# Performance work log

Measured on AMD Instinct MI355X. Metric: run time of the kernel, lower is better.

Reference implementation:

```python
import jax, jax.numpy as jnp
import numpy as np

B, H, W, C = 16, 32, 32, 512
L, CT = 77, 512
NH, HD = 8, 64
G = 32          # GroupNorm groups
EPS = 1e-6      # flax GroupNorm default epsilon
NEG = -1e10


def group_norm(x, scale, bias):
    # flax GroupNorm on [b, n, c]: stats over (n, channels-within-group) per (b, group)
    b, n, c = x.shape
    xg = x.reshape(b, n, G, c // G)
    mu = xg.mean(axis=(1, 3), keepdims=True)
    var = xg.var(axis=(1, 3), keepdims=True)
    xg = (xg - mu) * jax.lax.rsqrt(var + EPS)
    return xg.reshape(b, n, c) * scale + bias


def setup_inputs() -> dict:
    key = jax.random.key(0)
    ks = jax.random.split(key, 8)
    w = lambda k, shape: jax.random.normal(k, shape, jnp.float32) * 0.02
    return {
        "inputs": jax.random.normal(ks[0], (B, H, W, C), jnp.float32),
        "text_enc": jax.random.normal(ks[1], (B, L, CT), jnp.float32),
        "text_mask": jnp.ones((B, L), jnp.int32),
        "gn_q_scale": jnp.ones((C,), jnp.float32),
        "gn_q_bias": jnp.zeros((C,), jnp.float32),
        "gn_kv_scale": jnp.ones((C,), jnp.float32),
        "gn_kv_bias": jnp.zeros((C,), jnp.float32),
        "gn_t_scale": jnp.ones((CT,), jnp.float32),
        "gn_t_bias": jnp.zeros((CT,), jnp.float32),
        "Wq": w(ks[2], (C, NH, HD)),
        "Wk_self": w(ks[3], (C, NH, HD)),
        "Wv_self": w(ks[4], (C, NH, HD)),
        "Wk_cross": w(ks[5], (CT, NH, HD)),
        "Wv_cross": w(ks[6], (CT, NH, HD)),
        "Wout": w(ks[7], (NH, HD, C)),
    }


def reference(inputs, text_enc, text_mask,
              gn_q_scale, gn_q_bias, gn_kv_scale, gn_kv_bias,
              gn_t_scale, gn_t_bias,
              Wq, Wk_self, Wv_self, Wk_cross, Wv_cross, Wout):
    b, h, w, c = inputs.shape
    n = h * w
    x = inputs.reshape(b, n, c)

    x_q = group_norm(x, gn_q_scale, gn_q_bias)
    x_kv = group_norm(x, gn_kv_scale, gn_kv_bias)
    t = group_norm(text_enc, gn_t_scale, gn_t_bias)

    # q/k/v projections; fused: KV = concat(self-KV from image, cross-KV from text)
    scale = jnp.asarray(1.0 / np.sqrt(HD), inputs.dtype)
    q = jnp.einsum('bqc,chd->bqhd', x_q, Wq) * scale  # scale_attn_logits
    k = jnp.concatenate([jnp.einsum('bkc,chd->bkhd', x_kv, Wk_self),
                         jnp.einsum('blc,chd->blhd', t, Wk_cross)], axis=1)
    v = jnp.concatenate([jnp.einsum('bkc,chd->bkhd', x_kv, Wv_self),
                         jnp.einsum('blc,chd->blhd', t, Wv_cross)], axis=1)

    # make_attention_mask(ones[b,n], concat(ones[b,n], text_mask)) -> [b,1,n,n+l];
    # query mask is all ones so only the KV mask matters.
    kv_mask = jnp.concatenate(
        [jnp.ones((b, n), jnp.bool_), text_mask > 0], axis=1)  # [b, n+l]

    logits = jnp.einsum('bqhd,bkhd->bhqk', q, k)  # [b, nh, n, n+l]
    logits = jnp.where(kv_mask[:, None, None, :], logits, jnp.asarray(NEG, logits.dtype))
    probs = jax.nn.softmax(logits, axis=-1)
    attn = jnp.einsum('bhqk,bkhd->bqhd', probs, v)
    out = jnp.einsum('bqhd,hdc->bqc', attn, Wout)
    return out.reshape(b, h, w, c) + inputs
```

## Files before the change

kernel.cpp:

```cpp
#include <hip/hip_runtime.h>
#include <hip/hip_bf16.h>

typedef __hip_bfloat16 bf16;
typedef __attribute__((ext_vector_type(8))) short short8;
typedef __attribute__((ext_vector_type(4))) float f32x4;
typedef __attribute__((ext_vector_type(16))) float f32x16;
#define MFMA16(a, b, c) __builtin_amdgcn_mfma_f32_16x16x32_bf16(a, b, c, 0, 0, 0)
#define MFMA32(a, b, c) __builtin_amdgcn_mfma_f32_32x32x16_bf16(a, b, c, 0, 0, 0)

#define BB   16
#define CCH  512
#define NN   1024
#define LLT  77
#define LPAD 128
#define NHH  8
#define HDD  64
#define GGN  32
#define NKV  1101
#define KVP  1152

__device__ __forceinline__ unsigned short f2bu(float f){
  bf16 h = __float2bfloat16(f);
  return *reinterpret_cast<unsigned short*>(&h);
}

__device__ __forceinline__ unsigned pk2(float lo, float hi){
  unsigned r;
  asm("v_cvt_pk_bf16_f32 %0, %1, %2" : "=v"(r) : "v"(lo), "v"(hi));
  return r;
}

__device__ __forceinline__ float fexp2(float x){
  float r;
  asm("v_exp_f32 %0, %1" : "=v"(r) : "v"(x));
  return r;
}

__device__ __forceinline__ void pl32swap(unsigned &a, unsigned &b){
  asm("v_permlane32_swap_b32 %0, %1" : "+v"(a), "+v"(b));
}

__global__ __launch_bounds__(256) void gn_stats_kernel(
    const float* __restrict__ ximg, const float* __restrict__ xtxt,
    float* __restrict__ stats )
{
  int isimg = blockIdx.x < 512;
  int bid = blockIdx.x & 511;
  int b = bid >> 5, g = bid & 31;
  int npos = isimg ? NN : LLT;
  const float* xb = (isimg ? ximg : xtxt) + (size_t)b * npos * CCH + g * 16;
  int tot4 = npos * 4;
  float s = 0.f, s2 = 0.f;
  for (int e = threadIdx.x; e < tot4; e += 256){
    int n = e >> 2, cq = (e & 3) * 4;
    float4 v = *(const float4*)(xb + (size_t)n * CCH + cq);
    s  += v.x + v.y + v.z + v.w;
    s2 += v.x * v.x + v.y * v.y + v.z * v.z + v.w * v.w;
  }
  __shared__ float sh1[256], sh2[256];
  sh1[threadIdx.x] = s; sh2[threadIdx.x] = s2;
  __syncthreads();
  for (int off = 128; off > 0; off >>= 1){
    if (threadIdx.x < off){
      sh1[threadIdx.x] += sh1[threadIdx.x + off];
      sh2[threadIdx.x] += sh2[threadIdx.x + off];
    }
    __syncthreads();
  }
  if (threadIdx.x == 0){
    float inv = 1.f / (float)(npos * 16);
    float m = sh1[0] * inv;
    float var = sh2[0] * inv - m * m;
    float* mu = stats + (isimg ? 0 : 1024);
    mu[bid] = m;
    mu[512 + bid] = rsqrtf(var + 1e-6f);
  }
}

__global__ __launch_bounds__(256) void prep_weights_kernel(
    const float* __restrict__ W0, const float* __restrict__ W1,
    const float* __restrict__ W2, const float* __restrict__ W3,
    const float* __restrict__ W4, const float* __restrict__ W5,
    bf16* __restrict__ Wt)
{
  int wsel = blockIdx.z;
  const float* W = wsel == 0 ? W0 : wsel == 1 ? W1 : wsel == 2 ? W2 :
                   wsel == 3 ? W3 : wsel == 4 ? W4 : W5;
  bf16* dst = Wt + (size_t)wsel * CCH * CCH;
  int n0 = blockIdx.x * 64, k0 = blockIdx.y * 64;

  __shared__ alignas(16) float Ws[64][68];
  int r = threadIdx.x >> 2, c = (threadIdx.x & 3) * 16;
  const float* src = W + (size_t)(k0 + r) * CCH + n0 + c;
  *(float4*)&Ws[r][c]      = *(const float4*)(src);
  *(float4*)&Ws[r][c + 4]  = *(const float4*)(src + 4);
  *(float4*)&Ws[r][c + 8]  = *(const float4*)(src + 8);
  *(float4*)&Ws[r][c + 12] = *(const float4*)(src + 12);
  __syncthreads();

  int nr = threadIdx.x >> 2, kc = (threadIdx.x & 3) * 16;
  uint4 o0, o1;
  o0.x = pk2(Ws[kc + 0][nr],  Ws[kc + 1][nr]);
  o0.y = pk2(Ws[kc + 2][nr],  Ws[kc + 3][nr]);
  o0.z = pk2(Ws[kc + 4][nr],  Ws[kc + 5][nr]);
  o0.w = pk2(Ws[kc + 6][nr],  Ws[kc + 7][nr]);
  o1.x = pk2(Ws[kc + 8][nr],  Ws[kc + 9][nr]);
  o1.y = pk2(Ws[kc + 10][nr], Ws[kc + 11][nr]);
  o1.z = pk2(Ws[kc + 12][nr], Ws[kc + 13][nr]);
  o1.w = pk2(Ws[kc + 14][nr], Ws[kc + 15][nr]);
  bf16* d = dst + (size_t)(n0 + nr) * CCH + k0 + kc;
  *(uint4*)d = o0;
  *(uint4*)(d + 8) = o1;
}

__global__ __launch_bounds__(256) void norm_all_kernel(
    const float* __restrict__ x, const float* __restrict__ t,
    const float* __restrict__ stats,
    const float* __restrict__ gqs, const float* __restrict__ gqb,
    const float* __restrict__ gks, const float* __restrict__ gkb,
    const float* __restrict__ gts, const float* __restrict__ gtb,
    bf16* __restrict__ Xq, bf16* __restrict__ Xkv, bf16* __restrict__ Tn)
{
  if (blockIdx.x < 4096){
    size_t e = ((size_t)blockIdx.x * 256 + threadIdx.x) * 8;
    int b  = (int)(e >> 19);
    int ch = (int)(e & 511);
    int g  = ch >> 4;
    float m = stats[b * GGN + g], r = stats[512 + b * GGN + g];
    float4 x0 = *(const float4*)(x + e);
    float4 x1 = *(const float4*)(x + e + 4);
    float4 sq0 = *(const float4*)(gqs + ch), sq1 = *(const float4*)(gqs + ch + 4);
    float4 bq0 = *(const float4*)(gqb + ch), bq1 = *(const float4*)(gqb + ch + 4);
    float4 sk0 = *(const float4*)(gks + ch), sk1 = *(const float4*)(gks + ch + 4);
    float4 bk0 = *(const float4*)(gkb + ch), bk1 = *(const float4*)(gkb + ch + 4);
    float xs[8] = {x0.x,x0.y,x0.z,x0.w,x1.x,x1.y,x1.z,x1.w};
    float sqv[8] = {sq0.x,sq0.y,sq0.z,sq0.w,sq1.x,sq1.y,sq1.z,sq1.w};
    float bqv[8] = {bq0.x,bq0.y,bq0.z,bq0.w,bq1.x,bq1.y,bq1.z,bq1.w};
    float skv[8] = {sk0.x,sk0.y,sk0.z,sk0.w,sk1.x,sk1.y,sk1.z,sk1.w};
    float bkv[8] = {bk0.x,bk0.y,bk0.z,bk0.w,bk1.x,bk1.y,bk1.z,bk1.w};
    float q[8], k[8];
    #pragma unroll
    for (int j = 0; j < 8; j++){
      float nx = (xs[j] - m) * r;
      q[j] = (nx * sqv[j] + bqv[j]) * 0.18033688f;
      k[j] = nx * skv[j] + bkv[j];
    }
    uint4 oq, ok;
    oq.x = pk2(q[0], q[1]); oq.y = pk2(q[2], q[3]);
    oq.z = pk2(q[4], q[5]); oq.w = pk2(q[6], q[7]);
    ok.x = pk2(k[0], k[1]); ok.y = pk2(k[2], k[3]);
    ok.z = pk2(k[4], k[5]); ok.w = pk2(k[6], k[7]);
    *(uint4*)(Xq + e)  = oq;
    *(uint4*)(Xkv + e) = ok;
  } else {
    size_t e = ((size_t)(blockIdx.x - 4096) * 256 + threadIdx.x) * 8;
    int b  = (int)(e >> 16);
    int rem = (int)(e & 65535);
    int l  = rem >> 9;
    int ch = rem & 511;
    uint4 o;
    if (l < LLT){
      int g = ch >> 4;
      float m = stats[1024 + b * GGN + g], r = stats[1536 + b * GGN + g];
      const float* src = t + ((size_t)b * LLT + l) * CCH + ch;
      float4 x0 = *(const float4*)src, x1 = *(const float4*)(src + 4);
      float4 s0 = *(const float4*)(gts + ch), s1 = *(const float4*)(gts + ch + 4);
      float4 b0 = *(const float4*)(gtb + ch), b1 = *(const float4*)(gtb + ch + 4);
      float xs[8] = {x0.x,x0.y,x0.z,x0.w,x1.x,x1.y,x1.z,x1.w};
      float sv[8] = {s0.x,s0.y,s0.z,s0.w,s1.x,s1.y,s1.z,s1.w};
      float bv[8] = {b0.x,b0.y,b0.z,b0.w,b1.x,b1.y,b1.z,b1.w};
      float w[8];
      #pragma unroll
      for (int j = 0; j < 8; j++) w[j] = (xs[j] - m) * r * sv[j] + bv[j];
      o.x = pk2(w[0], w[1]); o.y = pk2(w[2], w[3]);
      o.z = pk2(w[4], w[5]); o.w = pk2(w[6], w[7]);
    } else {
      o = make_uint4(0, 0, 0, 0);
    }
    *(uint4*)(Tn + e) = o;
  }
}

__global__ __launch_bounds__(256) void proj_self_mfma(
    const bf16* __restrict__ Xq, const bf16* __restrict__ Xkv,
    const bf16* __restrict__ Wt,
    bf16* __restrict__ Qo, bf16* __restrict__ Ko, bf16* __restrict__ Vo)
{
  const int tid  = threadIdx.x;
  const int wave = tid >> 6, lane = tid & 63;
  const int l16 = lane & 15, quad = lane >> 4;
  const int wr = wave >> 1, wc = wave & 1;
  const int bx = blockIdx.x;
  const int ct = bx >> 7;
  const int rt = bx & 127;
  const int mat = ct >> 2;
  const int cm0 = (ct & 3) * 128;
  const int b  = rt >> 3;
  const int n0 = (rt & 7) * 128;

  __shared__ bf16 T[4][64][72];

  const bf16* A  = (mat == 0) ? Xq : Xkv;
  const bf16* Bw = Wt + (size_t)mat * CCH * CCH + (size_t)cm0 * CCH;

  f32x4 acc[4][4];
  #pragma unroll
  for (int rf = 0; rf < 4; rf++)
    #pragma unroll
    for (int cf = 0; cf < 4; cf++) acc[rf][cf] = (f32x4){0.f,0.f,0.f,0.f};

  const int sr = tid >> 2, sc = (tid & 3) * 16;
  const bf16* pa0 = A  + ((size_t)b * NN + n0 + sr) * CCH + sc;
  const bf16* pa1 = pa0 + (size_t)64 * CCH;
  const bf16* pb0 = Bw + (size_t)sr * CCH + sc;
  const bf16* pb1 = pb0 + (size_t)64 * CCH;

  uint4 rA0a = *(const uint4*)pa0, rA0b = *(const uint4*)(pa0 + 8);
  uint4 rA1a = *(const uint4*)pa1, rA1b = *(const uint4*)(pa1 + 8);
  uint4 rB0a = *(const uint4*)pb0, rB0b = *(const uint4*)(pb0 + 8);
  uint4 rB1a = *(const uint4*)pb1, rB1b = *(const uint4*)(pb1 + 8);

  for (int kt = 0; kt < 8; kt++){
    *(uint4*)&T[0][sr][sc] = rA0a;  *(uint4*)&T[0][sr][sc + 8] = rA0b;
    *(uint4*)&T[1][sr][sc] = rA1a;  *(uint4*)&T[1][sr][sc + 8] = rA1b;
    *(uint4*)&T[2][sr][sc] = rB0a;  *(uint4*)&T[2][sr][sc + 8] = rB0b;
    *(uint4*)&T[3][sr][sc] = rB1a;  *(uint4*)&T[3][sr][sc + 8] = rB1b;
    if (kt < 7){
      const int k1 = (kt + 1) * 64;
      rA0a = *(const uint4*)(pa0 + k1);  rA0b = *(const uint4*)(pa0 + k1 + 8);
      rA1a = *(const uint4*)(pa1 + k1);  rA1b = *(const uint4*)(pa1 + k1 + 8);
      rB0a = *(const uint4*)(pb0 + k1);  rB0b = *(const uint4*)(pb0 + k1 + 8);
      rB1a = *(const uint4*)(pb1 + k1);  rB1b = *(const uint4*)(pb1 + k1 + 8);
    }
    __syncthreads();

    short8 af[4][2];
    #pragma unroll
    for (int rf = 0; rf < 4; rf++){
      af[rf][0] = *(const short8*)&T[wr][rf * 16 + l16][quad * 8];
      af[rf][1] = *(const short8*)&T[wr][rf * 16 + l16][32 + quad * 8];
    }
    #pragma unroll
    for (int cf = 0; cf < 4; cf++){
      const short8 b0 = *(const short8*)&T[2 + wc][cf * 16 + l16][quad * 8];
      const short8 b1 = *(const short8*)&T[2 + wc][cf * 16 + l16][32 + quad * 8];
      #pragma unroll
      for (int rf = 0; rf < 4; rf++){
        acc[rf][cf] = MFMA16(af[rf][0], b0, acc[rf][cf]);
        acc[rf][cf] = MFMA16(af[rf][1], b1, acc[rf][cf]);
      }
    }
    __syncthreads();
  }

  if (mat < 2){
    bf16* Out = (mat == 0) ? Qo : Ko;
    const int stride = (mat == 0) ? NN : KVP;
    #pragma unroll
    for (int cf = 0; cf < 4; cf++){
      const int cm = cm0 + wc * 64 + cf * 16 + l16;
      const int h = cm >> 6, d = cm & 63;
      #pragma unroll
      for (int rf = 0; rf < 4; rf++)
        #pragma unroll
        for (int r = 0; r < 4; r++){
          const int n = n0 + wr * 64 + rf * 16 + quad * 4 + r;
          Out[(((size_t)b * NHH + h) * stride + n) * HDD + d] =
              __float2bfloat16(acc[rf][cf][r]);
        }
    }
  } else {
    bf16 (*Tw)[72] = T[wave];
    #pragma unroll
    for (int cf = 0; cf < 4; cf++)
      #pragma unroll
      for (int rf = 0; rf < 4; rf++)
        #pragma unroll
        for (int r = 0; r < 4; r++)
          Tw[cf * 16 + l16][rf * 16 + quad * 4 + r] =
              __float2bfloat16(acc[rf][cf][r]);
    __syncthreads();
    const int h  = (cm0 + wc * 64) >> 6;
    const int nb = n0 + wr * 64;
    const int dl = lane >> 2, cseg = (lane & 3) * 16;
    #pragma unroll
    for (int k2 = 0; k2 < 4; k2++){
      const int d = dl + k2 * 16;
      bf16* vd = Vo + (((size_t)b * NHH + h) * HDD + d) * KVP + nb + cseg;
      *(uint4*)vd       = *(const uint4*)&Tw[d][cseg];
      *(uint4*)(vd + 8) = *(const uint4*)&Tw[d][cseg + 8];
    }
  }
}

__global__ __launch_bounds__(256) void proj_cross_mfma(
    const bf16* __restrict__ Tn, const bf16* __restrict__ Wt,
    bf16* __restrict__ Ko, bf16* __restrict__ Vo)
{
  const int tid  = threadIdx.x;
  const int wave = tid >> 6, lane = tid & 63;
  const int l16 = lane & 15, quad = lane >> 4;
  const int h  = blockIdx.x;
  const int l0 = blockIdx.y * 64;
  const int b  = blockIdx.z;

  __shared__ bf16 At[64][72];
  __shared__ bf16 Bk[64][72], Bv[64][72];

  const bf16* Wkc = Wt + 3 * CCH * CCH;
  const bf16* Wvc = Wt + 4 * CCH * CCH;

  f32x4 sk[4], sv[4];
  #pragma unroll
  for (int nt = 0; nt < 4; nt++){
    sk[nt] = (f32x4){0.f,0.f,0.f,0.f};
    sv[nt] = (f32x4){0.f,0.f,0.f,0.f};
  }

  const int sr = tid >> 2, sc = (tid & 3) * 16;
  const bf16* p_a  = Tn  + ((size_t)b * LPAD + l0 + sr) * CCH + sc;
  const bf16* p_bk = Wkc + (size_t)(h * 64 + sr) * CCH + sc;
  const bf16* p_bv = Wvc + (size_t)(h * 64 + sr) * CCH + sc;

  uint4 ra0 = *(const uint4*)p_a,   ra1 = *(const uint4*)(p_a + 8);
  uint4 rk0 = *(const uint4*)p_bk,  rk1 = *(const uint4*)(p_bk + 8);
  uint4 rv0 = *(const uint4*)p_bv,  rv1 = *(const uint4*)(p_bv + 8);

  for (int kt = 0; kt < 8; kt++){
    *(uint4*)&At[sr][sc]     = ra0;  *(uint4*)&At[sr][sc + 8] = ra1;
    *(uint4*)&Bk[sr][sc]     = rk0;  *(uint4*)&Bk[sr][sc + 8] = rk1;
    *(uint4*)&Bv[sr][sc]     = rv0;  *(uint4*)&Bv[sr][sc + 8] = rv1;
    if (kt < 7){
      const int k1 = (kt + 1) * 64;
      ra0 = *(const uint4*)(p_a + k1);   ra1 = *(const uint4*)(p_a + k1 + 8);
      rk0 = *(const uint4*)(p_bk + k1);  rk1 = *(const uint4*)(p_bk + k1 + 8);
      rv0 = *(const uint4*)(p_bv + k1);  rv1 = *(const uint4*)(p_bv + k1 + 8);
    }
    __syncthreads();

    const short8 a0 = *(const short8*)&At[wave * 16 + l16][quad * 8];
    const short8 a1 = *(const short8*)&At[wave * 16 + l16][32 + quad * 8];
    #pragma unroll
    for (int nt = 0; nt < 4; nt++){
      const short8 bk0 = *(const short8*)&Bk[nt * 16 + l16][quad * 8];
      const short8 bk1 = *(const short8*)&Bk[nt * 16 + l16][32 + quad * 8];
      sk[nt] = MFMA16(a0, bk0, sk[nt]);
      sk[nt] = MFMA16(a1, bk1, sk[nt]);
      const short8 bv0 = *(const short8*)&Bv[nt * 16 + l16][quad * 8];
      const short8 bv1 = *(const short8*)&Bv[nt * 16 + l16][32 + quad * 8];
      sv[nt] = MFMA16(a0, bv0, sv[nt]);
      sv[nt] = MFMA16(a1, bv1, sv[nt]);
    }
    __syncthreads();
  }

  #pragma unroll
  for (int r = 0; r < 4; r++){
    int kvrow = NN + l0 + wave * 16 + quad * 4 + r;
    bf16* kd = Ko + (((size_t)b * NHH + h) * KVP + kvrow) * HDD + l16;
    #pragma unroll
    for (int nt = 0; nt < 4; nt++)
      kd[nt * 16] = __float2bfloat16(sk[nt][r]);
  }

  __syncthreads();
  #pragma unroll
  for (int nt = 0; nt < 4; nt++)
    #pragma unroll
    for (int r = 0; r < 4; r++)
      Bk[nt * 16 + l16][wave * 16 + quad * 4 + r] = __float2bfloat16(sv[nt][r]);
  __syncthreads();
  {
    int d = tid >> 2, c = (tid & 3) * 16;
    bf16* vd = Vo + (((size_t)b * NHH + h) * HDD + d) * KVP + NN + l0 + c;
    *(uint4*)vd       = *(const uint4*)&Bk[d][c];
    *(uint4*)(vd + 8) = *(const uint4*)&Bk[d][c + 8];
  }
}

__global__ __launch_bounds__(256, 4) void attn_mfma_kernel(
    const bf16* __restrict__ Q, const bf16* __restrict__ K,
    const bf16* __restrict__ Vt, const int* __restrict__ tmask,
    bf16* __restrict__ Ao)
{
  const int tid  = threadIdx.x;
  const int wave = tid >> 6;
  const int lane = tid & 63;
  const int l31  = lane & 31;
  const int hi   = lane >> 5;
  const int bx = blockIdx.x;
  const int q0 = (bx >> 7) * 128;
  const int g  = bx & 127;
  const int h  = g & 7;
  const int b  = g >> 3;

  __shared__ alignas(16) bf16 KV[2][2][64][72];

  const bf16* qp = Q + (((size_t)b * NHH + h) * NN + q0 + wave * 32 + l31) * HDD + hi * 8;
  short8 qf[4];
  qf[0] = *(const short8*)(qp);
  qf[1] = *(const short8*)(qp + 16);
  qf[2] = *(const short8*)(qp + 32);
  qf[3] = *(const short8*)(qp + 48);

  union { unsigned u[4]; short8 s8; } ones;
  ones.u[0] = 0x3F803F80u; ones.u[1] = 0x3F803F80u;
  ones.u[2] = 0x3F803F80u; ones.u[3] = 0x3F803F80u;

  f32x16 zf;
  #pragma unroll
  for (int i = 0; i < 16; i++) zf[i] = 0.f;

  f32x16 o_acc[2], l_acc;
  #pragma unroll
  for (int dt = 0; dt < 2; dt++)
    #pragma unroll
    for (int i = 0; i < 16; i++) o_acc[dt][i] = 0.f;
  #pragma unroll
  for (int i = 0; i < 16; i++) l_acc[i] = 0.f;

  const size_t kbase = ((size_t)b * NHH + h) * KVP;
  const size_t vbase = ((size_t)b * NHH + h) * (size_t)HDD * KVP;

  const int sr = tid >> 2;
  const int sc = (tid & 3) * 16;
  const bf16* kp = K  + (kbase + sr) * HDD + sc;
  const bf16* vp = Vt + vbase + (size_t)sr * KVP + sc;

  uint4 kr0 = *(const uint4*)kp, kr1 = *(const uint4*)(kp + 8);
  uint4 vr0 = *(const uint4*)vp, vr1 = *(const uint4*)(vp + 8);
  *(uint4*)&KV[0][0][sr][sc]     = kr0;
  *(uint4*)&KV[0][0][sr][sc + 8] = kr1;
  *(uint4*)&KV[0][1][sr][sc]     = vr0;
  *(uint4*)&KV[0][1][sr][sc + 8] = vr1;
  kr0 = *(const uint4*)(kp + 4096); kr1 = *(const uint4*)(kp + 4096 + 8);
  vr0 = *(const uint4*)(vp + 64);   vr1 = *(const uint4*)(vp + 64 + 8);
  __syncthreads();

  for (int kt = 0; kt < 18; kt++){
    const int cur = kt & 1;
    if (kt + 1 < 18){
      *(uint4*)&KV[cur ^ 1][0][sr][sc]     = kr0;
      *(uint4*)&KV[cur ^ 1][0][sr][sc + 8] = kr1;
      *(uint4*)&KV[cur ^ 1][1][sr][sc]     = vr0;
      *(uint4*)&KV[cur ^ 1][1][sr][sc + 8] = vr1;
    }
    if (kt + 2 < 18){
      const size_t ko = (size_t)(kt + 2) * 4096;
      const int    vo = (kt + 2) * 64;
      kr0 = *(const uint4*)(kp + ko); kr1 = *(const uint4*)(kp + ko + 8);
      vr0 = *(const uint4*)(vp + vo); vr1 = *(const uint4*)(vp + vo + 8);
    }

    const bf16 (*Ks)[72] = KV[cur][0];
    const bf16 (*Vs)[72] = KV[cur][1];
    const int kv0 = kt * 64;

    #pragma unroll
    for (int t = 0; t < 2; t++){
      const short8 kf0 = *(const short8*)&Ks[t * 32 + l31][hi * 8];
      const short8 kf1 = *(const short8*)&Ks[t * 32 + l31][16 + hi * 8];
      const short8 kf2 = *(const short8*)&Ks[t * 32 + l31][32 + hi * 8];
      const short8 kf3 = *(const short8*)&Ks[t * 32 + l31][48 + hi * 8];
      __builtin_amdgcn_s_setprio(1);
      f32x16 s = MFMA32(kf0, qf[0], zf);
      s = MFMA32(kf1, qf[1], s);
      s = MFMA32(kf2, qf[2], s);
      s = MFMA32(kf3, qf[3], s);
      __builtin_amdgcn_s_setprio(0);

      if (kv0 + 64 > NN){
        #pragma unroll
        for (int r = 0; r < 16; r++){
          int idx = kv0 - NN + t * 32 + (r & 3) + 8 * (r >> 2) + 4 * hi;
          int ci = idx < LLT ? idx : LLT - 1;
          float rep = (idx < LLT)
                        ? (tmask[b * LLT + ci] > 0 ? 1e30f : -1e10f)
                        : -1e30f;
          s[r] = fminf(s[r], rep);
        }
      }

      #pragma unroll
      for (int r = 0; r < 16; r++) s[r] = fexp2(s[r]);

      unsigned w0 = pk2(s[0],  s[1]),  w1 = pk2(s[2],  s[3]);
      unsigned w2 = pk2(s[4],  s[5]),  w3 = pk2(s[6],  s[7]);
      unsigned w4 = pk2(s[8],  s[9]),  w5 = pk2(s[10], s[11]);
      unsigned w6 = pk2(s[12], s[13]), w7 = pk2(s[14], s[15]);
      pl32swap(w0, w2);
      pl32swap(w1, w3);
      pl32swap(w4, w6);
      pl32swap(w5, w7);
      union { unsigned u[4]; short8 s8; } pf0, pf1;
      pf0.u[0] = w0; pf0.u[1] = w1; pf0.u[2] = w2; pf0.u[3] = w3;
      pf1.u[0] = w4; pf1.u[1] = w5; pf1.u[2] = w6; pf1.u[3] = w7;

      const short8 vf00 = *(const short8*)&Vs[l31][t * 32 + hi * 8];
      const short8 vf01 = *(const short8*)&Vs[l31][t * 32 + 16 + hi * 8];
      const short8 vf10 = *(const short8*)&Vs[32 + l31][t * 32 + hi * 8];
      const short8 vf11 = *(const short8*)&Vs[32 + l31][t * 32 + 16 + hi * 8];

      __builtin_amdgcn_s_setprio(1);
      l_acc = MFMA32(pf0.s8, ones.s8, l_acc);
      l_acc = MFMA32(pf1.s8, ones.s8, l_acc);
      o_acc[0] = MFMA32(pf0.s8, vf00, o_acc[0]);
      o_acc[0] = MFMA32(pf1.s8, vf01, o_acc[0]);
      o_acc[1] = MFMA32(pf0.s8, vf10, o_acc[1]);
      o_acc[1] = MFMA32(pf1.s8, vf11, o_acc[1]);
      __builtin_amdgcn_s_setprio(0);
    }
    __syncthreads();
  }

  #pragma unroll
  for (int r = 0; r < 16; r++){
    const int ql = (r & 3) + 8 * (r >> 2) + 4 * hi;
    const float linv = 1.f / l_acc[r];
    const int n = q0 + wave * 32 + ql;
    bf16* dst = Ao + ((size_t)b * NN + n) * CCH + h * HDD + l31;
    dst[0]  = __float2bfloat16(o_acc[0][r] * linv);
    dst[32] = __float2bfloat16(o_acc[1][r] * linv);
  }
}

__global__ __launch_bounds__(256) void outproj_mfma(
    const bf16* __restrict__ A, const bf16* __restrict__ Wt,
    const float* __restrict__ resid, float* __restrict__ out)
{
  const int tid  = threadIdx.x;
  const int wave = tid >> 6, lane = tid & 63;
  const int l16 = lane & 15, quad = lane >> 4;
  const int wr = wave >> 1, wc = wave & 1;
  const int bx = blockIdx.x;
  const int c0 = (bx >> 7) * 128;
  const int g0 = (bx & 127) * 128;

  __shared__ bf16 T[4][64][72];
  const bf16* Bw = Wt + (size_t)5 * CCH * CCH + (size_t)c0 * CCH;

  f32x4 acc[4][4];
  #pragma unroll
  for (int rf = 0; rf < 4; rf++)
    #pragma unroll
    for (int cf = 0; cf < 4; cf++) acc[rf][cf] = (f32x4){0.f,0.f,0.f,0.f};

  const int sr = tid >> 2, sc = (tid & 3) * 16;
  const bf16* pa0 = A  + ((size_t)g0 + sr) * CCH + sc;
  const bf16* pa1 = pa0 + (size_t)64 * CCH;
  const bf16* pb0 = Bw + (size_t)sr * CCH + sc;
  const bf16* pb1 = pb0 + (size_t)64 * CCH;

  uint4 rA0a = *(const uint4*)pa0, rA0b = *(const uint4*)(pa0 + 8);
  uint4 rA1a = *(const uint4*)pa1, rA1b = *(const uint4*)(pa1 + 8);
  uint4 rB0a = *(const uint4*)pb0, rB0b = *(const uint4*)(pb0 + 8);
  uint4 rB1a = *(const uint4*)pb1, rB1b = *(const uint4*)(pb1 + 8);

  for (int kt = 0; kt < 8; kt++){
    *(uint4*)&T[0][sr][sc] = rA0a;  *(uint4*)&T[0][sr][sc + 8] = rA0b;
    *(uint4*)&T[1][sr][sc] = rA1a;  *(uint4*)&T[1][sr][sc + 8] = rA1b;
    *(uint4*)&T[2][sr][sc] = rB0a;  *(uint4*)&T[2][sr][sc + 8] = rB0b;
    *(uint4*)&T[3][sr][sc] = rB1a;  *(uint4*)&T[3][sr][sc + 8] = rB1b;
    if (kt < 7){
      const int k1 = (kt + 1) * 64;
      rA0a = *(const uint4*)(pa0 + k1);  rA0b = *(const uint4*)(pa0 + k1 + 8);
      rA1a = *(const uint4*)(pa1 + k1);  rA1b = *(const uint4*)(pa1 + k1 + 8);
      rB0a = *(const uint4*)(pb0 + k1);  rB0b = *(const uint4*)(pb0 + k1 + 8);
      rB1a = *(const uint4*)(pb1 + k1);  rB1b = *(const uint4*)(pb1 + k1 + 8);
    }
    __syncthreads();

    short8 af[4][2];
    #pragma unroll
    for (int rf = 0; rf < 4; rf++){
      af[rf][0] = *(const short8*)&T[wr][rf * 16 + l16][quad * 8];
      af[rf][1] = *(const short8*)&T[wr][rf * 16 + l16][32 + quad * 8];
    }
    #pragma unroll
    for (int cf = 0; cf < 4; cf++){
      const short8 b0 = *(const short8*)&T[2 + wc][cf * 16 + l16][quad * 8];
      const short8 b1 = *(const short8*)&T[2 + wc][cf * 16 + l16][32 + quad * 8];
      #pragma unroll
      for (int rf = 0; rf < 4; rf++){
        acc[rf][cf] = MFMA16(af[rf][0], b0, acc[rf][cf]);
        acc[rf][cf] = MFMA16(af[rf][1], b1, acc[rf][cf]);
      }
    }
    __syncthreads();
  }

  #pragma unroll
  for (int rf = 0; rf < 4; rf++)
    #pragma unroll
    for (int r = 0; r < 4; r++){
      const size_t row = (size_t)g0 + wr * 64 + rf * 16 + quad * 4 + r;
      #pragma unroll
      for (int cf = 0; cf < 4; cf++){
        const int col = c0 + wc * 64 + cf * 16 + l16;
        out[row * CCH + col] = acc[rf][cf][r] + resid[row * CCH + col];
      }
    }
}

extern "C" void kernel_launch(void* const* d_in, const int* in_sizes, int n_in,
                              void* d_out, int out_size, void* d_ws, size_t ws_size,
                              hipStream_t stream)
{
  const float* x     = (const float*)d_in[0];
  const float* txt   = (const float*)d_in[1];
  const int*   tmask = (const int*)d_in[2];
  const float* gqs   = (const float*)d_in[3];
  const float* gqb   = (const float*)d_in[4];
  const float* gks   = (const float*)d_in[5];
  const float* gkb   = (const float*)d_in[6];
  const float* gts   = (const float*)d_in[7];
  const float* gtb   = (const float*)d_in[8];
  const float* Wq    = (const float*)d_in[9];
  const float* Wks   = (const float*)d_in[10];
  const float* Wvs   = (const float*)d_in[11];
  const float* Wkc   = (const float*)d_in[12];
  const float* Wvc   = (const float*)d_in[13];
  const float* Wout  = (const float*)d_in[14];

  float* stats = (float*)d_ws;
  bf16* WtAll = (bf16*)(stats + 2048);
  bf16* Xq  = WtAll + (size_t)6 * CCH * CCH;
  bf16* Xkv = Xq  + (size_t)BB * NN * CCH;
  bf16* Tn  = Xkv + (size_t)BB * NN * CCH;
  bf16* Qw  = Tn  + (size_t)BB * LPAD * CCH;
  bf16* Kw  = Qw  + (size_t)BB * NHH * NN * HDD;
  bf16* Vw  = Kw  + (size_t)BB * NHH * KVP * HDD;
  bf16* Aw  = Xq;

  gn_stats_kernel<<<1024, 256, 0, stream>>>(x, txt, stats);
  prep_weights_kernel<<<dim3(8, 8, 6), 256, 0, stream>>>(
      Wq, Wks, Wvs, Wkc, Wvc, Wout, WtAll);
  norm_all_kernel<<<4608, 256, 0, stream>>>(
      x, txt, stats, gqs, gqb, gks, gkb, gts, gtb, Xq, Xkv, Tn);
  proj_self_mfma<<<1536, 256, 0, stream>>>(
      Xq, Xkv, WtAll, Qw, Kw, Vw);
  proj_cross_mfma<<<dim3(8, 2, BB), 256, 0, stream>>>(
      Tn, WtAll, Kw, Vw);
  attn_mfma_kernel<<<1024, 256, 0, stream>>>(Qw, Kw, Vw, tmask, Aw);
  outproj_mfma<<<512, 256, 0, stream>>>(Aw, WtAll, x, (float*)d_out);
}
```

Measured before the change: 251.4 us.

## Merge small kernels and stage GEMM tiles via direct global-to-LDS loads

Folds the GroupNorm stats and weight-transpose kernels into one launch, and merges the self and cross projection kernels into one grid with block-index dispatch. The projection and output-projection GEMMs now load tiles with global_load_lds directly into unpadded LDS, replacing the register-staged prefetch. This aims to cut launch overhead and VGPR traffic. In exchange it loses the register double-buffering and the LDS padding, so bank conflicts on MFMA fragment reads may rise.

After: 241.9 us. 3.8% less time.

```diff
diff --git a/kernel.cpp b/kernel.cpp
--- a/kernel.cpp
+++ b/kernel.cpp
@@ -40,77 +40,86 @@
   asm("v_permlane32_swap_b32 %0, %1" : "+v"(a), "+v"(b));
 }
 
-__global__ __launch_bounds__(256) void gn_stats_kernel(
+__device__ __forceinline__ void gload16(const bf16* g, bf16* l){
+  __builtin_amdgcn_global_load_lds(
+      (const __attribute__((address_space(1))) unsigned int*)g,
+      (__attribute__((address_space(3))) unsigned int*)l,
+      16, 0, 0);
+}
+
+__global__ __launch_bounds__(256) void pre_kernel(
     const float* __restrict__ ximg, const float* __restrict__ xtxt,
-    float* __restrict__ stats )
-{
-  int isimg = blockIdx.x < 512;
-  int bid = blockIdx.x & 511;
-  int b = bid >> 5, g = bid & 31;
-  int npos = isimg ? NN : LLT;
-  const float* xb = (isimg ? ximg : xtxt) + (size_t)b * npos * CCH + g * 16;
-  int tot4 = npos * 4;
-  float s = 0.f, s2 = 0.f;
-  for (int e = threadIdx.x; e < tot4; e += 256){
-    int n = e >> 2, cq = (e & 3) * 4;
-    float4 v = *(const float4*)(xb + (size_t)n * CCH + cq);
-    s  += v.x + v.y + v.z + v.w;
-    s2 += v.x * v.x + v.y * v.y + v.z * v.z + v.w * v.w;
-  }
-  __shared__ float sh1[256], sh2[256];
-  sh1[threadIdx.x] = s; sh2[threadIdx.x] = s2;
-  __syncthreads();
-  for (int off = 128; off > 0; off >>= 1){
-    if (threadIdx.x < off){
-      sh1[threadIdx.x] += sh1[threadIdx.x + off];
-      sh2[threadIdx.x] += sh2[threadIdx.x + off];
-    }
-    __syncthreads();
-  }
-  if (threadIdx.x == 0){
-    float inv = 1.f / (float)(npos * 16);
-    float m = sh1[0] * inv;
-    float var = sh2[0] * inv - m * m;
-    float* mu = stats + (isimg ? 0 : 1024);
-    mu[bid] = m;
-    mu[512 + bid] = rsqrtf(var + 1e-6f);
-  }
-}
-
-__global__ __launch_bounds__(256) void prep_weights_kernel(
+    float* __restrict__ stats,
     const float* __restrict__ W0, const float* __restrict__ W1,
     const float* __restrict__ W2, const float* __restrict__ W3,
     const float* __restrict__ W4, const float* __restrict__ W5,
     bf16* __restrict__ Wt)
 {
-  int wsel = blockIdx.z;
-  const float* W = wsel == 0 ? W0 : wsel == 1 ? W1 : wsel == 2 ? W2 :
-                   wsel == 3 ? W3 : wsel == 4 ? W4 : W5;
-  bf16* dst = Wt + (size_t)wsel * CCH * CCH;
-  int n0 = blockIdx.x * 64, k0 = blockIdx.y * 64;
-
+  __shared__ float sh1[256], sh2[256];
   __shared__ alignas(16) float Ws[64][68];
-  int r = threadIdx.x >> 2, c = (threadIdx.x & 3) * 16;
-  const float* src = W + (size_t)(k0 + r) * CCH + n0 + c;
-  *(float4*)&Ws[r][c]      = *(const float4*)(src);
-  *(float4*)&Ws[r][c + 4]  = *(const float4*)(src + 4);
-  *(float4*)&Ws[r][c + 8]  = *(const float4*)(src + 8);
-  *(float4*)&Ws[r][c + 12] = *(const float4*)(src + 12);
-  __syncthreads();
-
-  int nr = threadIdx.x >> 2, kc = (threadIdx.x & 3) * 16;
-  uint4 o0, o1;
-  o0.x = pk2(Ws[kc + 0][nr],  Ws[kc + 1][nr]);
-  o0.y = pk2(Ws[kc + 2][nr],  Ws[kc + 3][nr]);
-  o0.z = pk2(Ws[kc + 4][nr],  Ws[kc + 5][nr]);
-  o0.w = pk2(Ws[kc + 6][nr],  Ws[kc + 7][nr]);
-  o1.x = pk2(Ws[kc + 8][nr],  Ws[kc + 9][nr]);
-  o1.y = pk2(Ws[kc + 10][nr], Ws[kc + 11][nr]);
-  o1.z = pk2(Ws[kc + 12][nr], Ws[kc + 13][nr]);
-  o1.w = pk2(Ws[kc + 14][nr], Ws[kc + 15][nr]);
-  bf16* d = dst + (size_t)(n0 + nr) * CCH + k0 + kc;
-  *(uint4*)d = o0;
-  *(uint4*)(d + 8) = o1;
+
+  if (blockIdx.x < 1024){
+    int isimg = blockIdx.x < 512;
+    int bid = blockIdx.x & 511;
+    int b = bid >> 5, g = bid & 31;
+    int npos = isimg ? NN : LLT;
+    const float* xb = (isimg ? ximg : xtxt) + (size_t)b * npos * CCH + g * 16;
+    int tot4 = npos * 4;
+    float s = 0.f, s2 = 0.f;
+    for (int e = threadIdx.x; e < tot4; e += 256){
+      int n = e >> 2, cq = (e & 3) * 4;
+      float4 v = *(const float4*)(xb + (size_t)n * CCH + cq);
+      s  += v.x + v.y + v.z + v.w;
+      s2 += v.x * v.x + v.y * v.y + v.z * v.z + v.w * v.w;
+    }
+    sh1[threadIdx.x] = s; sh2[threadIdx.x] = s2;
+    __syncthreads();
+    for (int off = 128; off > 0; off >>= 1){
+      if (threadIdx.x < off){
+        sh1[threadIdx.x] += sh1[threadIdx.x + off];
+        sh2[threadIdx.x] += sh2[threadIdx.x + off];
+      }
+      __syncthreads();
+    }
+    if (threadIdx.x == 0){
+      float inv = 1.f / (float)(npos * 16);
+      float m = sh1[0] * inv;
+      float var = sh2[0] * inv - m * m;
+      float* mu = stats + (isimg ? 0 : 1024);
+      mu[bid] = m;
+      mu[512 + bid] = rsqrtf(var + 1e-6f);
+    }
+  } else {
+    int i = blockIdx.x - 1024;
+    int wsel = i >> 6;
+    int rem  = i & 63;
+    int n0 = (rem & 7) * 64, k0 = (rem >> 3) * 64;
+    const float* W = wsel == 0 ? W0 : wsel == 1 ? W1 : wsel == 2 ? W2 :
+                     wsel == 3 ? W3 : wsel == 4 ? W4 : W5;
+    bf16* dst = Wt + (size_t)wsel * CCH * CCH;
+
+    int r = threadIdx.x >> 2, c = (threadIdx.x & 3) * 16;
+    const float* src = W + (size_t)(k0 + r) * CCH + n0 + c;
+    *(float4*)&Ws[r][c]      = *(const float4*)(src);
+    *(float4*)&Ws[r][c + 4]  = *(const float4*)(src + 4);
+    *(float4*)&Ws[r][c + 8]  = *(const float4*)(src + 8);
+    *(float4*)&Ws[r][c + 12] = *(const float4*)(src + 12);
+    __syncthreads();
+
+    int nr = threadIdx.x >> 2, kc = (threadIdx.x & 3) * 16;
+    uint4 o0, o1;
+    o0.x = pk2(Ws[kc + 0][nr],  Ws[kc + 1][nr]);
+    o0.y = pk2(Ws[kc + 2][nr],  Ws[kc + 3][nr]);
+    o0.z = pk2(Ws[kc + 4][nr],  Ws[kc + 5][nr]);
+    o0.w = pk2(Ws[kc + 6][nr],  Ws[kc + 7][nr]);
+    o1.x = pk2(Ws[kc + 8][nr],  Ws[kc + 9][nr]);
+    o1.y = pk2(Ws[kc + 10][nr], Ws[kc + 11][nr]);
+    o1.z = pk2(Ws[kc + 12][nr], Ws[kc + 13][nr]);
+    o1.w = pk2(Ws[kc + 14][nr], Ws[kc + 15][nr]);
+    bf16* d = dst + (size_t)(n0 + nr) * CCH + k0 + kc;
+    *(uint4*)d = o0;
+    *(uint4*)(d + 8) = o1;
+  }
 }
 
 __global__ __launch_bounds__(256) void norm_all_kernel(
@@ -181,200 +190,185 @@
   }
 }
 
-__global__ __launch_bounds__(256) void proj_self_mfma(
+__global__ __launch_bounds__(256) void proj_all_mfma(
     const bf16* __restrict__ Xq, const bf16* __restrict__ Xkv,
-    const bf16* __restrict__ Wt,
+    const bf16* __restrict__ Tn, const bf16* __restrict__ Wt,
     bf16* __restrict__ Qo, bf16* __restrict__ Ko, bf16* __restrict__ Vo)
 {
+  __shared__ alignas(16) char SHRAW[36864];
   const int tid  = threadIdx.x;
   const int wave = tid >> 6, lane = tid & 63;
   const int l16 = lane & 15, quad = lane >> 4;
-  const int wr = wave >> 1, wc = wave & 1;
   const int bx = blockIdx.x;
-  const int ct = bx >> 7;
-  const int rt = bx & 127;
-  const int mat = ct >> 2;
-  const int cm0 = (ct & 3) * 128;
-  const int b  = rt >> 3;
-  const int n0 = (rt & 7) * 128;
-
-  __shared__ bf16 T[4][64][72];
-
-  const bf16* A  = (mat == 0) ? Xq : Xkv;
-  const bf16* Bw = Wt + (size_t)mat * CCH * CCH + (size_t)cm0 * CCH;
-
-  f32x4 acc[4][4];
-  #pragma unroll
-  for (int rf = 0; rf < 4; rf++)
-    #pragma unroll
-    for (int cf = 0; cf < 4; cf++) acc[rf][cf] = (f32x4){0.f,0.f,0.f,0.f};
-
-  const int sr = tid >> 2, sc = (tid & 3) * 16;
-  const bf16* pa0 = A  + ((size_t)b * NN + n0 + sr) * CCH + sc;
-  const bf16* pa1 = pa0 + (size_t)64 * CCH;
-  const bf16* pb0 = Bw + (size_t)sr * CCH + sc;
-  const bf16* pb1 = pb0 + (size_t)64 * CCH;
-
-  uint4 rA0a = *(const uint4*)pa0, rA0b = *(const uint4*)(pa0 + 8);
-  uint4 rA1a = *(const uint4*)pa1, rA1b = *(const uint4*)(pa1 + 8);
-  uint4 rB0a = *(const uint4*)pb0, rB0b = *(const uint4*)(pb0 + 8);
-  uint4 rB1a = *(const uint4*)pb1, rB1b = *(const uint4*)(pb1 + 8);
-
-  for (int kt = 0; kt < 8; kt++){
-    *(uint4*)&T[0][sr][sc] = rA0a;  *(uint4*)&T[0][sr][sc + 8] = rA0b;
-    *(uint4*)&T[1][sr][sc] = rA1a;  *(uint4*)&T[1][sr][sc + 8] = rA1b;
-    *(uint4*)&T[2][sr][sc] = rB0a;  *(uint4*)&T[2][sr][sc + 8] = rB0b;
-    *(uint4*)&T[3][sr][sc] = rB1a;  *(uint4*)&T[3][sr][sc + 8] = rB1b;
-    if (kt < 7){
-      const int k1 = (kt + 1) * 64;
-      rA0a = *(const uint4*)(pa0 + k1);  rA0b = *(const uint4*)(pa0 + k1 + 8);
-      rA1a = *(const uint4*)(pa1 + k1);  rA1b = *(const uint4*)(pa1 + k1 + 8);
-      rB0a = *(const uint4*)(pb0 + k1);  rB0b = *(const uint4*)(pb0 + k1 + 8);
-      rB1a = *(const uint4*)(pb1 + k1);  rB1b = *(const uint4*)(pb1 + k1 + 8);
-    }
+
+  if (bx < 1536){
+    bf16 (*T)[64][64] = reinterpret_cast<bf16(*)[64][64]>(SHRAW);
+    const int wr = wave >> 1, wc = wave & 1;
+    const int ct = bx >> 7;
+    const int rt = bx & 127;
+    const int mat = ct >> 2;
+    const int cm0 = (ct & 3) * 128;
+    const int b  = rt >> 3;
+    const int n0 = (rt & 7) * 128;
+
+    const bf16* A  = (mat == 0) ? Xq : Xkv;
+    const bf16* Bw = Wt + (size_t)mat * CCH * CCH + (size_t)cm0 * CCH;
+
+    f32x4 acc[4][4];
+    #pragma unroll
+    for (int rf = 0; rf < 4; rf++)
+      #pragma unroll
+      for (int cf = 0; cf < 4; cf++) acc[rf][cf] = (f32x4){0.f,0.f,0.f,0.f};
+
+    const int lrow = lane >> 3, lcol = (lane & 7) * 8;
+    const bf16* srcbase = (wave < 2)
+        ? A  + ((size_t)b * NN + n0 + wave * 64) * CCH
+        : Bw + (size_t)((wave - 2) * 64) * CCH;
+
+    for (int kt = 0; kt < 8; kt++){
+      const int kc = kt * 64;
+      #pragma unroll
+      for (int c = 0; c < 8; c++){
+        const bf16* g = srcbase + (size_t)(c * 8 + lrow) * CCH + kc + lcol;
+        gload16(g, &T[wave][c * 8][0]);
+      }
+      __syncthreads();
+
+      short8 af[4][2];
+      #pragma unroll
+      for (int rf = 0; rf < 4; rf++){
+        af[rf][0] = *(const short8*)&T[wr][rf * 16 + l16][quad * 8];
+        af[rf][1] = *(const short8*)&T[wr][rf * 16 + l16][32 + quad * 8];
+      }
+      #pragma unroll
+      for (int cf = 0; cf < 4; cf++){
+        const short8 b0 = *(const short8*)&T[2 + wc][cf * 16 + l16][quad * 8];
+        const short8 b1 = *(const short8*)&T[2 + wc][cf * 16 + l16][32 + quad * 8];
+        #pragma unroll
+        for (int rf = 0; rf < 4; rf++){
+          acc[rf][cf] = MFMA16(af[rf][0], b0, acc[rf][cf]);
+          acc[rf][cf] = MFMA16(af[rf][1], b1, acc[rf][cf]);
+        }
+      }
+      __syncthreads();
+    }
+
+    if (mat < 2){
+      bf16* Out = (mat == 0) ? Qo : Ko;
+      const int stride = (mat == 0) ? NN : KVP;
+      #pragma unroll
+      for (int cf = 0; cf < 4; cf++){
+        const int cm = cm0 + wc * 64 + cf * 16 + l16;
+        const int h = cm >> 6, d = cm & 63;
+        #pragma unroll
+        for (int rf = 0; rf < 4; rf++)
+          #pragma unroll
+          for (int r = 0; r < 4; r++){
+            const int n = n0 + wr * 64 + rf * 16 + quad * 4 + r;
+            Out[(((size_t)b * NHH + h) * stride + n) * HDD + d] =
+                __float2bfloat16(acc[rf][cf][r]);
+          }
+      }
+    } else {
+      bf16 (*Tw)[64] = T[wave];
+      #pragma unroll
+      for (int cf = 0; cf < 4; cf++)
+        #pragma unroll
+        for (int rf = 0; rf < 4; rf++)
+          #pragma unroll
+          for (int r = 0; r < 4; r++)
+            Tw[cf * 16 + l16][rf * 16 + quad * 4 + r] =
+                __float2bfloat16(acc[rf][cf][r]);
+      __syncthreads();
+      const int h  = (cm0 + wc * 64) >> 6;
+      const int nb = n0 + wr * 64;
+      const int dl = lane >> 2, cseg = (lane & 3) * 16;
+      #pragma unroll
+      for (int k2 = 0; k2 < 4; k2++){
+        const int d = dl + k2 * 16;
+        bf16* vd = Vo + (((size_t)b * NHH + h) * HDD + d) * KVP + nb + cseg;
+        *(uint4*)vd       = *(const uint4*)&Tw[d][cseg];
+        *(uint4*)(vd + 8) = *(const uint4*)&Tw[d][cseg + 8];
+      }
+    }
+  } else {
+    bf16 (*At)[72] = reinterpret_cast<bf16(*)[72]>(SHRAW);
+    bf16 (*Bk)[72] = reinterpret_cast<bf16(*)[72]>(SHRAW + 64 * 72 * 2);
+    bf16 (*Bv)[72] = reinterpret_cast<bf16(*)[72]>(SHRAW + 2 * 64 * 72 * 2);
+    const int i  = bx - 1536;
+    const int h  = i & 7;
+    const int l0 = ((i >> 3) & 1) * 64;
+    const int b  = i >> 4;
+
+    const bf16* Wkc = Wt + 3 * CCH * CCH;
+    const bf16* Wvc = Wt + 4 * CCH * CCH;
+
+    f32x4 sk[4], sv[4];
+    #pragma unroll
+    for (int nt = 0; nt < 4; nt++){
+      sk[nt] = (f32x4){0.f,0.f,0.f,0.f};
+      sv[nt] = (f32x4){0.f,0.f,0.f,0.f};
+    }
+
+    const int sr = tid >> 2, sc = (tid & 3) * 16;
+    const bf16* p_a  = Tn  + ((size_t)b * LPAD + l0 + sr) * CCH + sc;
+    const bf16* p_bk = Wkc + (size_t)(h * 64 + sr) * CCH + sc;
+    const bf16* p_bv = Wvc + (size_t)(h * 64 + sr) * CCH + sc;
+
+    uint4 ra0 = *(const uint4*)p_a,   ra1 = *(const uint4*)(p_a + 8);
+    uint4 rk0 = *(const uint4*)p_bk,  rk1 = *(const uint4*)(p_bk + 8);
+    uint4 rv0 = *(const uint4*)p_bv,  rv1 = *(const uint4*)(p_bv + 8);
+
+    for (int kt = 0; kt < 8; kt++){
+      *(uint4*)&At[sr][sc]     = ra0;  *(uint4*)&At[sr][sc + 8] = ra1;
+      *(uint4*)&Bk[sr][sc]     = rk0;  *(uint4*)&Bk[sr][sc + 8] = rk1;
+      *(uint4*)&Bv[sr][sc]     = rv0;  *(uint4*)&Bv[sr][sc + 8] = rv1;
+      if (kt < 7){
+        const int k1 = (kt + 1) * 64;
+        ra0 = *(const uint4*)(p_a + k1);   ra1 = *(const uint4*)(p_a + k1 + 8);
+        rk0 = *(const uint4*)(p_bk + k1);  rk1 = *(const uint4*)(p_bk + k1 + 8);
+        rv0 = *(const uint4*)(p_bv + k1);  rv1 = *(const uint4*)(p_bv + k1 + 8);
+      }
+      __syncthreads();
+
+      const short8 a0 = *(const short8*)&At[wave * 16 + l16][quad * 8];
+      const short8 a1 = *(const short8*)&At[wave * 16 + l16][32 + quad * 8];
+      #pragma unroll
+      for (int nt = 0; nt < 4; nt++){
+        const short8 bk0 = *(const short8*)&Bk[nt * 16 + l16][quad * 8];
+        const short8 bk1 = *(const short8*)&Bk[nt * 16 + l16][32 + quad * 8];
+        sk[nt] = MFMA16(a0, bk0, sk[nt]);
+        sk[nt] = MFMA16(a1, bk1, sk[nt]);
+        const short8 bv0 = *(const short8*)&Bv[nt * 16 + l16][quad * 8];
+        const short8 bv1 = *(const short8*)&Bv[nt * 16 + l16][32 + quad * 8];
+        sv[nt] = MFMA16(a0, bv0, sv[nt]);
+        sv[nt] = MFMA16(a1, bv1, sv[nt]);
+      }
+      __syncthreads();
+    }
+
+    #pragma unroll
+    for (int r = 0; r < 4; r++){
+      int kvrow = NN + l0 + wave * 16 + quad * 4 + r;
+      bf16* kd = Ko + (((size_t)b * NHH + h) * KVP + kvrow) * HDD + l16;
+      #pragma unroll
+      for (int nt = 0; nt < 4; nt++)
+        kd[nt * 16] = __float2bfloat16(sk[nt][r]);
+    }
+
     __syncthreads();
-
-    short8 af[4][2];
-    #pragma unroll
-    for (int rf = 0; rf < 4; rf++){
-      af[rf][0] = *(const short8*)&T[wr][rf * 16 + l16][quad * 8];
-      af[rf][1] = *(const short8*)&T[wr][rf * 16 + l16][32 + quad * 8];
-    }
-    #pragma unroll
-    for (int cf = 0; cf < 4; cf++){
-      const short8 b0 = *(const short8*)&T[2 + wc][cf * 16 + l16][quad * 8];
-      const short8 b1 = *(const short8*)&T[2 + wc][cf * 16 + l16][32 + quad * 8];
-      #pragma unroll
-      for (int rf = 0; rf < 4; rf++){
-        acc[rf][cf] = MFMA16(af[rf][0], b0, acc[rf][cf]);
-        acc[rf][cf] = MFMA16(af[rf][1], b1, acc[rf][cf]);
-      }
-    }
+    #pragma unroll
+    for (int nt = 0; nt < 4; nt++)
+      #pragma unroll
+      for (int r = 0; r < 4; r++)
+        Bk[nt * 16 + l16][wave * 16 + quad * 4 + r] = __float2bfloat16(sv[nt][r]);
     __syncthreads();
-  }
-
-  if (mat < 2){
-    bf16* Out = (mat == 0) ? Qo : Ko;
-    const int stride = (mat == 0) ? NN : KVP;
-    #pragma unroll
-    for (int cf = 0; cf < 4; cf++){
-      const int cm = cm0 + wc * 64 + cf * 16 + l16;
-      const int h = cm >> 6, d = cm & 63;
-      #pragma unroll
-      for (int rf = 0; rf < 4; rf++)
-        #pragma unroll
-        for (int r = 0; r < 4; r++){
-          const int n = n0 + wr * 64 + rf * 16 + quad * 4 + r;
-          Out[(((size_t)b * NHH + h) * stride + n) * HDD + d] =
-              __float2bfloat16(acc[rf][cf][r]);
-        }
-    }
-  } else {
-    bf16 (*Tw)[72] = T[wave];
-    #pragma unroll
-    for (int cf = 0; cf < 4; cf++)
-      #pragma unroll
-      for (int rf = 0; rf < 4; rf++)
-        #pragma unroll
-        for (int r = 0; r < 4; r++)
-          Tw[cf * 16 + l16][rf * 16 + quad * 4 + r] =
-              __float2bfloat16(acc[rf][cf][r]);
-    __syncthreads();
-    const int h  = (cm0 + wc * 64) >> 6;
-    const int nb = n0 + wr * 64;
-    const int dl = lane >> 2, cseg = (lane & 3) * 16;
-    #pragma unroll
-    for (int k2 = 0; k2 < 4; k2++){
-      const int d = dl + k2 * 16;
-      bf16* vd = Vo + (((size_t)b * NHH + h) * HDD + d) * KVP + nb + cseg;
-      *(uint4*)vd       = *(const uint4*)&Tw[d][cseg];
-      *(uint4*)(vd + 8) = *(const uint4*)&Tw[d][cseg + 8];
-    }
-  }
-}
-
-__global__ __launch_bounds__(256) void proj_cross_mfma(
-    const bf16* __restrict__ Tn, const bf16* __restrict__ Wt,
-    bf16* __restrict__ Ko, bf16* __restrict__ Vo)
-{
-  const int tid  = threadIdx.x;
-  const int wave = tid >> 6, lane = tid & 63;
-  const int l16 = lane & 15, quad = lane >> 4;
-  const int h  = blockIdx.x;
-  const int l0 = blockIdx.y * 64;
-  const int b  = blockIdx.z;
-
-  __shared__ bf16 At[64][72];
-  __shared__ bf16 Bk[64][72], Bv[64][72];
-
-  const bf16* Wkc = Wt + 3 * CCH * CCH;
-  const bf16* Wvc = Wt + 4 * CCH * CCH;
-
-  f32x4 sk[4], sv[4];
-  #pragma unroll
-  for (int nt = 0; nt < 4; nt++){
-    sk[nt] = (f32x4){0.f,0.f,0.f,0.f};
-    sv[nt] = (f32x4){0.f,0.f,0.f,0.f};
-  }
-
-  const int sr = tid >> 2, sc = (tid & 3) * 16;
-  const bf16* p_a  = Tn  + ((size_t)b * LPAD + l0 + sr) * CCH + sc;
-  const bf16* p_bk = Wkc + (size_t)(h * 64 + sr) * CCH + sc;
-  const bf16* p_bv = Wvc + (size_t)(h * 64 + sr) * CCH + sc;
-
-  uint4 ra0 = *(const uint4*)p_a,   ra1 = *(const uint4*)(p_a + 8);
-  uint4 rk0 = *(const uint4*)p_bk,  rk1 = *(const uint4*)(p_bk + 8);
-  uint4 rv0 = *(const uint4*)p_bv,  rv1 = *(const uint4*)(p_bv + 8);
-
-  for (int kt = 0; kt < 8; kt++){
-    *(uint4*)&At[sr][sc]     = ra0;  *(uint4*)&At[sr][sc + 8] = ra1;
-    *(uint4*)&Bk[sr][sc]     = rk0;  *(uint4*)&Bk[sr][sc + 8] = rk1;
-    *(uint4*)&Bv[sr][sc]     = rv0;  *(uint4*)&Bv[sr][sc + 8] = rv1;
-    if (kt < 7){
-      const int k1 = (kt + 1) * 64;
-      ra0 = *(const uint4*)(p_a + k1);   ra1 = *(const uint4*)(p_a + k1 + 8);
-      rk0 = *(const uint4*)(p_bk + k1);  rk1 = *(const uint4*)(p_bk + k1 + 8);
-      rv0 = *(const uint4*)(p_bv + k1);  rv1 = *(const uint4*)(p_bv + k1 + 8);
-    }
-    __syncthreads();
-
-    const short8 a0 = *(const short8*)&At[wave * 16 + l16][quad * 8];
-    const short8 a1 = *(const short8*)&At[wave * 16 + l16][32 + quad * 8];
-    #pragma unroll
-    for (int nt = 0; nt < 4; nt++){
-      const short8 bk0 = *(const short8*)&Bk[nt * 16 + l16][quad * 8];
-      const short8 bk1 = *(const short8*)&Bk[nt * 16 + l16][32 + quad * 8];
-      sk[nt] = MFMA16(a0, bk0, sk[nt]);
-      sk[nt] = MFMA16(a1, bk1, sk[nt]);
-      const short8 bv0 = *(const short8*)&Bv[nt * 16 + l16][quad * 8];
-      const short8 bv1 = *(const short8*)&Bv[nt * 16 + l16][32 + quad * 8];
-      sv[nt] = MFMA16(a0, bv0, sv[nt]);
-      sv[nt] = MFMA16(a1, bv1, sv[nt]);
-    }
-    __syncthreads();
-  }
-
-  #pragma unroll
-  for (int r = 0; r < 4; r++){
-    int kvrow = NN + l0 + wave * 16 + quad * 4 + r;
-    bf16* kd = Ko + (((size_t)b * NHH + h) * KVP + kvrow) * HDD + l16;
-    #pragma unroll
-    for (int nt = 0; nt < 4; nt++)
-      kd[nt * 16] = __float2bfloat16(sk[nt][r]);
-  }
-
-  __syncthreads();
-  #pragma unroll
-  for (int nt = 0; nt < 4; nt++)
-    #pragma unroll
-    for (int r = 0; r < 4; r++)
-      Bk[nt * 16 + l16][wave * 16 + quad * 4 + r] = __float2bfloat16(sv[nt][r]);
-  __syncthreads();
-  {
-    int d = tid >> 2, c = (tid & 3) * 16;
-    bf16* vd = Vo + (((size_t)b * NHH + h) * HDD + d) * KVP + NN + l0 + c;
-    *(uint4*)vd       = *(const uint4*)&Bk[d][c];
-    *(uint4*)(vd + 8) = *(const uint4*)&Bk[d][c + 8];
+    {
+      int d = tid >> 2, c = (tid & 3) * 16;
+      bf16* vd = Vo + (((size_t)b * NHH + h) * HDD + d) * KVP + NN + l0 + c;
+      *(uint4*)vd       = *(const uint4*)&Bk[d][c];
+      *(uint4*)(vd + 8) = *(const uint4*)&Bk[d][c + 8];
+    }
   }
 }
 
@@ -528,6 +522,7 @@
     const bf16* __restrict__ A, const bf16* __restrict__ Wt,
     const float* __restrict__ resid, float* __restrict__ out)
 {
+  __shared__ alignas(16) bf16 T[4][64][64];
   const int tid  = threadIdx.x;
   const int wave = tid >> 6, lane = tid & 63;
   const int l16 = lane & 15, quad = lane >> 4;
@@ -536,7 +531,6 @@
   const int c0 = (bx >> 7) * 128;
   const int g0 = (bx & 127) * 128;
 
-  __shared__ bf16 T[4][64][72];
   const bf16* Bw = Wt + (size_t)5 * CCH * CCH + (size_t)c0 * CCH;
 
   f32x4 acc[4][4];
@@ -545,28 +539,17 @@
     #pragma unroll
     for (int cf = 0; cf < 4; cf++) acc[rf][cf] = (f32x4){0.f,0.f,0.f,0.f};
 
-  const int sr = tid >> 2, sc = (tid & 3) * 16;
-  const bf16* pa0 = A  + ((size_t)g0 + sr) * CCH + sc;
-  const bf16* pa1 = pa0 + (size_t)64 * CCH;
-  const bf16* pb0 = Bw + (size_t)sr * CCH + sc;
-  const bf16* pb1 = pb0 + (size_t)64 * CCH;
-
-  uint4 rA0a = *(const uint4*)pa0, rA0b = *(const uint4*)(pa0 + 8);
-  uint4 rA1a = *(const uint4*)pa1, rA1b = *(const uint4*)(pa1 + 8);
-  uint4 rB0a = *(const uint4*)pb0, rB0b = *(const uint4*)(pb0 + 8);
-  uint4 rB1a = *(const uint4*)pb1, rB1b = *(const uint4*)(pb1 + 8);
+  const int lrow = lane >> 3, lcol = (lane & 7) * 8;
+  const bf16* srcbase = (wave < 2)
+      ? A  + ((size_t)g0 + wave * 64) * CCH
+      : Bw + (size_t)((wave - 2) * 64) * CCH;
 
   for (int kt = 0; kt < 8; kt++){
-    *(uint4*)&T[0][sr][sc] = rA0a;  *(uint4*)&T[0][sr][sc + 8] = rA0b;
-    *(uint4*)&T[1][sr][sc] = rA1a;  *(uint4*)&T[1][sr][sc + 8] = rA1b;
-    *(uint4*)&T[2][sr][sc] = rB0a;  *(uint4*)&T[2][sr][sc + 8] = rB0b;
-    *(uint4*)&T[3][sr][sc] = rB1a;  *(uint4*)&T[3][sr][sc + 8] = rB1b;
-    if (kt < 7){
-      const int k1 = (kt + 1) * 64;
-      rA0a = *(const uint4*)(pa0 + k1);  rA0b = *(const uint4*)(pa0 + k1 + 8);
-      rA1a = *(const uint4*)(pa1 + k1);  rA1b = *(const uint4*)(pa1 + k1 + 8);
-      rB0a = *(const uint4*)(pb0 + k1);  rB0b = *(const uint4*)(pb0 + k1 + 8);
-      rB1a = *(const uint4*)(pb1 + k1);  rB1b = *(const uint4*)(pb1 + k1 + 8);
+    const int kc = kt * 64;
+    #pragma unroll
+    for (int c = 0; c < 8; c++){
+      const bf16* g = srcbase + (size_t)(c * 8 + lrow) * CCH + kc + lcol;
+      gload16(g, &T[wave][c * 8][0]);
     }
     __syncthreads();
 
@@ -632,15 +615,12 @@
   bf16* Vw  = Kw  + (size_t)BB * NHH * KVP * HDD;
   bf16* Aw  = Xq;
 
-  gn_stats_kernel<<<1024, 256, 0, stream>>>(x, txt, stats);
-  prep_weights_kernel<<<dim3(8, 8, 6), 256, 0, stream>>>(
-      Wq, Wks, Wvs, Wkc, Wvc, Wout, WtAll);
+  pre_kernel<<<1408, 256, 0, stream>>>(
+      x, txt, stats, Wq, Wks, Wvs, Wkc, Wvc, Wout, WtAll);
   norm_all_kernel<<<4608, 256, 0, stream>>>(
       x, txt, stats, gqs, gqb, gks, gkb, gts, gtb, Xq, Xkv, Tn);
-  proj_self_mfma<<<1536, 256, 0, stream>>>(
-      Xq, Xkv, WtAll, Qw, Kw, Vw);
-  proj_cross_mfma<<<dim3(8, 2, BB), 256, 0, stream>>>(
-      Tn, WtAll, Kw, Vw);
+  proj_all_mfma<<<1792, 256, 0, stream>>>(
+      Xq, Xkv, Tn, WtAll, Qw, Kw, Vw);
   attn_mfma_kernel<<<1024, 256, 0, stream>>>(Qw, Kw, Vw, tmask, Aw);
   outproj_mfma<<<512, 256, 0, stream>>>(Aw, WtAll, x, (float*)d_out);
 }
```
